# Optimization experiments

Hardware: AMD Instinct MI355X
Metric: run time of the kernel (lower is better)

## Reference

```python
import jax, jax.numpy as jnp
import numpy as np

NUM_EXPERTS = 8
TOP_K = 2
B, S, H = 4, 1024, 1024
FF = 2 * H  # expert hidden = 2*hidden_size per the torch code


def setup_inputs() -> dict:
    key = jax.random.key(0)
    ks = jax.random.split(key, 5)
    scale = 0.02
    return {
        "x": jax.random.normal(ks[0], (B, S, H), dtype=jnp.float32),
        "Wg": jax.random.normal(ks[1], (H, NUM_EXPERTS), dtype=jnp.float32) * scale,
        "bg": jnp.zeros((NUM_EXPERTS,), dtype=jnp.float32),
        "W1": jax.random.normal(ks[2], (NUM_EXPERTS, H, FF), dtype=jnp.float32) * scale,
        "b1": jnp.zeros((NUM_EXPERTS, FF), dtype=jnp.float32),
        "W2": jax.random.normal(ks[3], (NUM_EXPERTS, FF, H), dtype=jnp.float32) * scale,
        "b2": jnp.zeros((NUM_EXPERTS, H), dtype=jnp.float32),
    }


def reference(x, Wg, bg, W1, b1, W2, b2):
    b, s, h = x.shape
    xf = x.reshape(-1, h)  # [T, H]
    # Gating: softmax over experts, then top-k and renormalize (as in torch code)
    gate_scores = jax.nn.softmax(xf @ Wg + bg, axis=-1)  # [T, E]
    top_v, top_i = jax.lax.top_k(gate_scores, TOP_K)      # [T, K]
    top_v = top_v / jnp.sum(top_v, axis=-1, keepdims=True)
    # Combine weights per (token, expert): gate if expert selected else 0
    combine = jnp.sum(jax.nn.one_hot(top_i, NUM_EXPERTS, dtype=xf.dtype)
                      * top_v[..., None], axis=1)         # [T, E]
    # Dense all-expert MLP (eval-mode dropout = identity), then gated combine
    hmid = jax.nn.relu(jnp.einsum('th,ehf->tef', xf, W1) + b1)  # [T, E, FF]
    yexp = jnp.einsum('tef,efh->teh', hmid, W2) + b2            # [T, E, H]
    out = jnp.einsum('te,teh->th', combine, yexp)               # [T, H]
    return out.reshape(b, s, h)
```

## Files before the change

kernel.cpp:

```cpp
#include <hip/hip_runtime.h>
#include <hip/hip_bf16.h>

#define T_TOK 4096
#define HD    1024
#define FFD   2048
#define NE    8

typedef __attribute__((ext_vector_type(8))) short short8;
typedef __attribute__((ext_vector_type(4))) float f32x4;

__device__ __forceinline__ unsigned short f2bf(float f) {
  __hip_bfloat16 h = __float2bfloat16(f);
  return __builtin_bit_cast(unsigned short, h);
}

__device__ __forceinline__ void gload_lds16(const unsigned short* g, unsigned short* l) {
  __builtin_amdgcn_global_load_lds(
      (const __attribute__((address_space(1))) unsigned int*)g,
      (__attribute__((address_space(3))) unsigned int*)l, 16, 0, 0);
}

__global__ __launch_bounds__(256) void prep_kernel(
    const float* __restrict__ x, const float* __restrict__ Wg,
    const float* __restrict__ bg,
    const float* __restrict__ W1, const float* __restrict__ W2,
    int* __restrict__ top_i, float2* __restrict__ top_w,
    unsigned short* __restrict__ xbf,
    unsigned short* __restrict__ W1T, unsigned short* __restrict__ W2T,
    float* __restrict__ out)
{
  __shared__ float tile[64][69];
  const int bid = blockIdx.x;
  const int tid = threadIdx.x;

  if (bid < T_TOK / 4) {
    {
      size_t b = ((size_t)bid * 256 + tid) * 16;
      float4 z = make_float4(0.f, 0.f, 0.f, 0.f);
#pragma unroll
      for (int q = 0; q < 4; ++q) *(float4*)(out + b + q * 4) = z;
    }
    const int wave = tid >> 6;
    const int lane = tid & 63;
    const int t = bid * 4 + wave;

    float acc[NE];
#pragma unroll
    for (int e = 0; e < NE; ++e) acc[e] = 0.f;

    const float* xr = x + (size_t)t * HD;
    unsigned short* xo = xbf + (size_t)t * HD;
#pragma unroll
    for (int it = 0; it < 4; ++it) {
      const int h0 = lane * 4 + it * 256;
      float4 xv = *(const float4*)(xr + h0);
#pragma unroll
      for (int j = 0; j < 4; ++j) {
        float xs = (&xv.x)[j];
        float4 a = *(const float4*)(Wg + (size_t)(h0 + j) * NE);
        float4 b = *(const float4*)(Wg + (size_t)(h0 + j) * NE + 4);
        acc[0] = fmaf(xs, a.x, acc[0]); acc[1] = fmaf(xs, a.y, acc[1]);
        acc[2] = fmaf(xs, a.z, acc[2]); acc[3] = fmaf(xs, a.w, acc[3]);
        acc[4] = fmaf(xs, b.x, acc[4]); acc[5] = fmaf(xs, b.y, acc[5]);
        acc[6] = fmaf(xs, b.z, acc[6]); acc[7] = fmaf(xs, b.w, acc[7]);
      }
      ushort4 u;
      u.x = f2bf(xv.x); u.y = f2bf(xv.y); u.z = f2bf(xv.z); u.w = f2bf(xv.w);
      *(ushort4*)(xo + h0) = u;
    }
#pragma unroll
    for (int off = 32; off > 0; off >>= 1) {
#pragma unroll
      for (int e = 0; e < NE; ++e) acc[e] += __shfl_xor(acc[e], off);
    }
    if (lane == 0) {
      float lg[NE];
#pragma unroll
      for (int e = 0; e < NE; ++e) lg[e] = acc[e] + bg[e];
      int i1 = 0;
#pragma unroll
      for (int e = 1; e < NE; ++e) if (lg[e] > lg[i1]) i1 = e;
      int i2 = (i1 == 0) ? 1 : 0;
#pragma unroll
      for (int e = 0; e < NE; ++e) if (e != i1 && lg[e] > lg[i2]) i2 = e;
      float p2 = expf(lg[i2] - lg[i1]);
      float s  = 1.f + p2;
      top_i[t] = i1 | (i2 << 8);
      top_w[t] = make_float2(1.f / s, p2 / s);
    }
    return;
  }

  const float* in; unsigned short* ow; int R, C, idx;
  if (bid < T_TOK / 4 + 4096) {
    idx = bid - T_TOK / 4;          in = W1; ow = W1T; R = HD;  C = FFD;
  } else {
    idx = bid - (T_TOK / 4 + 4096); in = W2; ow = W2T; R = FFD; C = HD;
  }
  const int cpt = C >> 6, rpt = R >> 6;
  const int cx = idx % cpt;
  const int cy = (idx / cpt) % rpt;
  const int z  = idx / (cpt * rpt);
  const int r0 = cy * 64, c0 = cx * 64;

  const float* ip = in + ((size_t)z * R + r0) * C + c0;
  int tr = tid >> 4, tc = (tid & 15) * 4;
#pragma unroll
  for (int j = 0; j < 4; ++j) {
    float4 v = *(const float4*)(ip + (size_t)(tr + j * 16) * C + tc);
    float* tp = &tile[tr + j * 16][tc];
    tp[0] = v.x; tp[1] = v.y; tp[2] = v.z; tp[3] = v.w;
  }
  __syncthreads();
  unsigned short* op = ow + ((size_t)z * C + c0) * R + r0;
  int oc = tid >> 4, orr = (tid & 15) * 4;
#pragma unroll
  for (int j = 0; j < 4; ++j) {
    int c = oc + j * 16;
    ushort4 w;
    w.x = f2bf(tile[orr + 0][c]);
    w.y = f2bf(tile[orr + 1][c]);
    w.z = f2bf(tile[orr + 2][c]);
    w.w = f2bf(tile[orr + 3][c]);
    *(ushort4*)(op + (size_t)c * R + orr) = w;
  }
}

__global__ __launch_bounds__(256) void route_kernel(
    const int* __restrict__ top_i, const float2* __restrict__ top_w,
    int* __restrict__ counts, int* __restrict__ ids, float* __restrict__ wts)
{
  const int e   = blockIdx.x;
  const int tid = threadIdx.x;
  __shared__ int psum[256];

  const int t0 = tid * 16;
  unsigned int flags = 0;
  int cnt = 0;
#pragma unroll
  for (int j = 0; j < 16; ++j) {
    int ti = top_i[t0 + j];
    bool m = ((ti & 255) == e) || (((ti >> 8) & 255) == e);
    flags |= (m ? 1u : 0u) << j;
    cnt += m;
  }
  psum[tid] = cnt;
  __syncthreads();
  for (int off = 1; off < 256; off <<= 1) {
    int v = (tid >= off) ? psum[tid - off] : 0;
    __syncthreads();
    psum[tid] += v;
    __syncthreads();
  }
  int rank = psum[tid] - cnt;
#pragma unroll
  for (int j = 0; j < 16; ++j) {
    if (flags & (1u << j)) {
      int t = t0 + j;
      int ti = top_i[t];
      float2 w = top_w[t];
      ids[e * T_TOK + rank] = t;
      wts[e * T_TOK + rank] = ((ti & 255) == e) ? w.x : w.y;
      ++rank;
    }
  }
  if (tid == 255) counts[e] = psum[255];
}

template<int KD, int ND, int KSPLIT, bool G1M, bool GATHER_A>
__global__ __launch_bounds__(256, 4) void pair_gemm128_kernel(
    const unsigned short* __restrict__ A,
    const unsigned short* __restrict__ BT,
    const float* __restrict__ bias,
    const int* __restrict__ counts, const int* __restrict__ ids,
    const float* __restrict__ wts,
    unsigned short* __restrict__ Hout, float* __restrict__ out)
{
  constexpr int CT    = ND / 128;
  constexpr int KTILE = KD / KSPLIT;
  constexpr int NT    = KTILE / 64;
  constexpr int SPX   = 128;

  const int e  = blockIdx.x & 7;
  const int s0 = blockIdx.x >> 3;
  int cnt = 0, base = 0;
#pragma unroll
  for (int k = 0; k < NE; ++k) {
    int c = counts[k];
    if (k < e)  base += (c + 255) & ~255;
    if (k == e) cnt = c;
  }
  const int ntiles = (cnt + 127) >> 7;
  const int njobs  = ntiles * CT * KSPLIT;

  __shared__ __align__(16) unsigned short As[128 * 64];
  __shared__ __align__(16) unsigned short Bs[128 * 64];

  const int tid  = threadIdx.x;
  const int w    = tid >> 6;
  const int lane = tid & 63;
  const int g    = lane >> 4;
  const int rA   = lane & 15;
  const int wr   = w >> 1;
  const int wc   = w & 1;
  const int sw   = rA & 7;
  const int srow = lane >> 3;
  const int lc8  = ((lane & 7) ^ srow) * 8;

  for (int slot = s0; slot < njobs; slot += SPX) {
    const int rt   = slot % ntiles;
    const int ct   = (slot / ntiles) % CT;
    const int kp   = slot / (ntiles * CT);
    const int row0 = base + rt * 128;
    const int koff = kp * KTILE;

    const unsigned short* arow[4];
#pragma unroll
    for (int jj = 0; jj < 4; ++jj) {
      const int lrow = w * 32 + jj * 8 + srow;
      int src;
      if constexpr (GATHER_A) {
        int i = rt * 128 + lrow;
        src = ids[e * T_TOK + (i < cnt ? i : cnt - 1)];
      } else {
        src = row0 + lrow;
      }
      arow[jj] = A + (size_t)src * KD + koff + lc8;
    }
    const unsigned short* Bb =
        BT + ((size_t)e * ND + (size_t)ct * 128) * KD + koff + lc8;

    f32x4 acc[4][4];
#pragma unroll
    for (int mf = 0; mf < 4; ++mf)
#pragma unroll
      for (int nf = 0; nf < 4; ++nf)
        acc[mf][nf] = (f32x4){0.f, 0.f, 0.f, 0.f};

    for (int kc = 0; kc < KTILE; kc += 64) {
      __syncthreads();
#pragma unroll
      for (int jj = 0; jj < 4; ++jj) {
        const int rg = w * 32 + jj * 8;
        gload_lds16(arow[jj] + kc, &As[rg * 64]);
        gload_lds16(Bb + (size_t)(rg + srow) * KD + kc, &Bs[rg * 64]);
      }
      __syncthreads();
#pragma unroll
      for (int ks = 0; ks < 2; ++ks) {
        const int pc = ((ks * 4 + g) ^ sw) << 3;
        short8 af[4], bf[4];
#pragma unroll
        for (int mf = 0; mf < 4; ++mf)
          af[mf] = *(const short8*)&As[(wr * 64 + mf * 16 + rA) * 64 + pc];
#pragma unroll
        for (int nf = 0; nf < 4; ++nf)
          bf[nf] = *(const short8*)&Bs[(wc * 64 + nf * 16 + rA) * 64 + pc];
#pragma unroll
        for (int mf = 0; mf < 4; ++mf)
#pragma unroll
          for (int nf = 0; nf < 4; ++nf)
            acc[mf][nf] = __builtin_amdgcn_mfma_f32_16x16x32_bf16(
                af[mf], bf[nf], acc[mf][nf], 0, 0, 0);
      }
    }

    float bv[4];
#pragma unroll
    for (int nf = 0; nf < 4; ++nf)
      bv[nf] = (KSPLIT == 1 || kp == 0)
                   ? bias[e * ND + ct * 128 + wc * 64 + nf * 16 + rA] : 0.f;

    if constexpr (G1M) {
#pragma unroll
      for (int mf = 0; mf < 4; ++mf)
#pragma unroll
        for (int r = 0; r < 4; ++r) {
          const int row = row0 + wr * 64 + mf * 16 + g * 4 + r;
          unsigned short* hrow =
              Hout + (size_t)row * FFD + ct * 128 + wc * 64 + rA;
#pragma unroll
          for (int nf = 0; nf < 4; ++nf)
            hrow[nf * 16] = f2bf(fmaxf(acc[mf][nf][r] + bv[nf], 0.f));
        }
    } else {
#pragma unroll
      for (int mf = 0; mf < 4; ++mf)
#pragma unroll
        for (int r = 0; r < 4; ++r) {
          const int i = rt * 128 + wr * 64 + mf * 16 + g * 4 + r;
          if (i >= cnt) continue;
          const int tok = ids[e * T_TOK + i];
          const float wt = wts[e * T_TOK + i];
          float* orow = out + (size_t)tok * HD + ct * 128 + wc * 64 + rA;
#pragma unroll
          for (int nf = 0; nf < 4; ++nf)
            atomicAdd(&orow[nf * 16], wt * (acc[mf][nf][r] + bv[nf]));
        }
    }
  }
}

extern "C" void kernel_launch(void* const* d_in, const int* in_sizes, int n_in,
                              void* d_out, int out_size, void* d_ws, size_t ws_size,
                              hipStream_t stream) {
  const float* x  = (const float*)d_in[0];
  const float* Wg = (const float*)d_in[1];
  const float* bg = (const float*)d_in[2];
  const float* W1 = (const float*)d_in[3];
  const float* b1 = (const float*)d_in[4];
  const float* W2 = (const float*)d_in[5];
  const float* b2 = (const float*)d_in[6];
  float* out = (float*)d_out;

  const size_t OFF_TOPI = 512;
  const size_t OFF_TOPW = OFF_TOPI + (size_t)T_TOK * 4;
  const size_t OFF_IDS  = OFF_TOPW + (size_t)T_TOK * 8;
  const size_t OFF_WTS  = OFF_IDS + (size_t)T_TOK * NE * 4;
  const size_t OFF_XBF  = OFF_WTS + (size_t)T_TOK * NE * 4;
  const size_t OFF_W1T  = OFF_XBF + (size_t)T_TOK * HD * 2;
  const size_t OFF_W2T  = OFF_W1T + (size_t)NE * HD * FFD * 2;
  const size_t OFF_H    = OFF_W2T + (size_t)NE * HD * FFD * 2;
  const size_t REQ      = OFF_H + (size_t)10240 * FFD * 2;

  if (ws_size < REQ) return;

  int*            counts = (int*)d_ws;
  int*            top_i  = (int*)((char*)d_ws + OFF_TOPI);
  float2*         top_w  = (float2*)((char*)d_ws + OFF_TOPW);
  int*            ids    = (int*)((char*)d_ws + OFF_IDS);
  float*          wts    = (float*)((char*)d_ws + OFF_WTS);
  unsigned short* xbf    = (unsigned short*)((char*)d_ws + OFF_XBF);
  unsigned short* W1T    = (unsigned short*)((char*)d_ws + OFF_W1T);
  unsigned short* W2T    = (unsigned short*)((char*)d_ws + OFF_W2T);
  unsigned short* H      = (unsigned short*)((char*)d_ws + OFF_H);

  prep_kernel<<<T_TOK / 4 + 2 * 4096, 256, 0, stream>>>(
      x, Wg, bg, W1, W2, top_i, top_w, xbf, W1T, W2T, out);
  route_kernel<<<NE, 256, 0, stream>>>(top_i, top_w, counts, ids, wts);

  pair_gemm128_kernel<HD, FFD, 1, true, true>
      <<<NE * 128, 256, 0, stream>>>(xbf, W1T, b1, counts, ids, wts, H, nullptr);
  pair_gemm128_kernel<FFD, HD, 2, false, false>
      <<<NE * 128, 256, 0, stream>>>(H, W2T, b2, counts, ids, wts, nullptr, out);
}
```

Before: 192.2 us.

## Use 256x128 tiles with 512 threads and double-buffered LDS prefetch

The expert GEMM kernel now uses 512-thread blocks computing 256x128 output tiles, one job per block instead of a persistent grid-stride loop. LDS is double-buffered so the next K-slice's global-to-LDS loads are issued before the current slice's MFMAs, with a single barrier per iteration. The larger tile reuses each B tile across more rows, reducing global traffic, and the prefetch overlaps load latency with compute. In exchange, padding waste grows for experts whose token count is not a multiple of 256, LDS use rises to 96 KB per block, and occupancy falls to 2 blocks per CU.

```diff
diff --git a/kernel.cpp b/kernel.cpp
--- a/kernel.cpp
+++ b/kernel.cpp
@@ -168,7 +168,7 @@
 }
 
 template<int KD, int ND, int KSPLIT, bool G1M, bool GATHER_A>
-__global__ __launch_bounds__(256, 4) void pair_gemm128_kernel(
+__global__ __launch_bounds__(512, 2) void pair_gemm256_kernel(
     const unsigned short* __restrict__ A,
     const unsigned short* __restrict__ BT,
     const float* __restrict__ bias,
@@ -179,10 +179,9 @@
   constexpr int CT    = ND / 128;
   constexpr int KTILE = KD / KSPLIT;
   constexpr int NT    = KTILE / 64;
-  constexpr int SPX   = 128;
-
-  const int e  = blockIdx.x & 7;
-  const int s0 = blockIdx.x >> 3;
+
+  const int e    = blockIdx.x & 7;
+  const int slot = blockIdx.x >> 3;
   int cnt = 0, base = 0;
 #pragma unroll
   for (int k = 0; k < NE; ++k) {
@@ -190,11 +189,16 @@
     if (k < e)  base += (c + 255) & ~255;
     if (k == e) cnt = c;
   }
-  const int ntiles = (cnt + 127) >> 7;
-  const int njobs  = ntiles * CT * KSPLIT;
-
-  __shared__ __align__(16) unsigned short As[128 * 64];
-  __shared__ __align__(16) unsigned short Bs[128 * 64];
+  const int ntiles = (cnt + 255) >> 8;
+  if (slot >= ntiles * CT * KSPLIT) return;
+  const int rt   = slot % ntiles;
+  const int ct   = (slot / ntiles) % CT;
+  const int kp   = slot / (ntiles * CT);
+  const int row0 = base + rt * 256;
+  const int koff = kp * KTILE;
+
+  __shared__ __align__(16) unsigned short As[2][256 * 64];
+  __shared__ __align__(16) unsigned short Bs[2][128 * 64];
 
   const int tid  = threadIdx.x;
   const int w    = tid >> 6;
@@ -207,97 +211,106 @@
   const int srow = lane >> 3;
   const int lc8  = ((lane & 7) ^ srow) * 8;
 
-  for (int slot = s0; slot < njobs; slot += SPX) {
-    const int rt   = slot % ntiles;
-    const int ct   = (slot / ntiles) % CT;
-    const int kp   = slot / (ntiles * CT);
-    const int row0 = base + rt * 128;
-    const int koff = kp * KTILE;
-
-    const unsigned short* arow[4];
-#pragma unroll
-    for (int jj = 0; jj < 4; ++jj) {
-      const int lrow = w * 32 + jj * 8 + srow;
-      int src;
-      if constexpr (GATHER_A) {
-        int i = rt * 128 + lrow;
-        src = ids[e * T_TOK + (i < cnt ? i : cnt - 1)];
-      } else {
-        src = row0 + lrow;
+  const unsigned short* arow[4];
+#pragma unroll
+  for (int jj = 0; jj < 4; ++jj) {
+    const int lrow = w * 32 + jj * 8 + srow;
+    int src;
+    if constexpr (GATHER_A) {
+      int i = rt * 256 + lrow;
+      src = ids[e * T_TOK + (i < cnt ? i : cnt - 1)];
+    } else {
+      src = row0 + lrow;
+    }
+    arow[jj] = A + (size_t)src * KD + koff + lc8;
+  }
+  const unsigned short* brow[2];
+#pragma unroll
+  for (int jj = 0; jj < 2; ++jj) {
+    const int lrow = w * 16 + jj * 8 + srow;
+    brow[jj] = BT + ((size_t)e * ND + ct * 128 + lrow) * KD + koff + lc8;
+  }
+
+  f32x4 acc[4][4];
+#pragma unroll
+  for (int mf = 0; mf < 4; ++mf)
+#pragma unroll
+    for (int nf = 0; nf < 4; ++nf)
+      acc[mf][nf] = (f32x4){0.f, 0.f, 0.f, 0.f};
+
+  auto stage = [&](int buf, int kc) {
+#pragma unroll
+    for (int jj = 0; jj < 4; ++jj)
+      gload_lds16(arow[jj] + kc, &As[buf][(w * 32 + jj * 8) * 64]);
+#pragma unroll
+    for (int jj = 0; jj < 2; ++jj)
+      gload_lds16(brow[jj] + kc, &Bs[buf][(w * 16 + jj * 8) * 64]);
+  };
+
+  stage(0, 0);
+  asm volatile("s_waitcnt vmcnt(0)" ::: "memory");
+  __builtin_amdgcn_s_barrier();
+
+#pragma unroll 2
+  for (int t = 0; t < NT; ++t) {
+    const int cur = t & 1;
+    if (t + 1 < NT) stage(cur ^ 1, (t + 1) * 64);
+    __builtin_amdgcn_sched_barrier(0);
+
+#pragma unroll
+    for (int ks = 0; ks < 2; ++ks) {
+      const int pc = ((ks * 4 + g) ^ sw) << 3;
+      short8 bf[4];
+#pragma unroll
+      for (int nf = 0; nf < 4; ++nf)
+        bf[nf] = *(const short8*)&Bs[cur][(wc * 64 + nf * 16 + rA) * 64 + pc];
+#pragma unroll
+      for (int mf = 0; mf < 4; ++mf) {
+        short8 af = *(const short8*)&As[cur][(wr * 64 + mf * 16 + rA) * 64 + pc];
+#pragma unroll
+        for (int nf = 0; nf < 4; ++nf)
+          acc[mf][nf] = __builtin_amdgcn_mfma_f32_16x16x32_bf16(
+              af, bf[nf], acc[mf][nf], 0, 0, 0);
       }
-      arow[jj] = A + (size_t)src * KD + koff + lc8;
-    }
-    const unsigned short* Bb =
-        BT + ((size_t)e * ND + (size_t)ct * 128) * KD + koff + lc8;
-
-    f32x4 acc[4][4];
+    }
+
+    asm volatile("s_waitcnt lgkmcnt(0) vmcnt(0)" ::: "memory");
+    __builtin_amdgcn_sched_barrier(0);
+    __builtin_amdgcn_s_barrier();
+    __builtin_amdgcn_sched_barrier(0);
+  }
+
+  float bv[4];
+#pragma unroll
+  for (int nf = 0; nf < 4; ++nf)
+    bv[nf] = (KSPLIT == 1 || kp == 0)
+                 ? bias[e * ND + ct * 128 + wc * 64 + nf * 16 + rA] : 0.f;
+
+  if constexpr (G1M) {
 #pragma unroll
     for (int mf = 0; mf < 4; ++mf)
 #pragma unroll
-      for (int nf = 0; nf < 4; ++nf)
-        acc[mf][nf] = (f32x4){0.f, 0.f, 0.f, 0.f};
-
-    for (int kc = 0; kc < KTILE; kc += 64) {
-      __syncthreads();
-#pragma unroll
-      for (int jj = 0; jj < 4; ++jj) {
-        const int rg = w * 32 + jj * 8;
-        gload_lds16(arow[jj] + kc, &As[rg * 64]);
-        gload_lds16(Bb + (size_t)(rg + srow) * KD + kc, &Bs[rg * 64]);
+      for (int r = 0; r < 4; ++r) {
+        const int row = row0 + wr * 64 + mf * 16 + g * 4 + r;
+        unsigned short* hrow = Hout + (size_t)row * FFD + ct * 128 + wc * 64 + rA;
+#pragma unroll
+        for (int nf = 0; nf < 4; ++nf)
+          hrow[nf * 16] = f2bf(fmaxf(acc[mf][nf][r] + bv[nf], 0.f));
       }
-      __syncthreads();
-#pragma unroll
-      for (int ks = 0; ks < 2; ++ks) {
-        const int pc = ((ks * 4 + g) ^ sw) << 3;
-        short8 af[4], bf[4];
-#pragma unroll
-        for (int mf = 0; mf < 4; ++mf)
-          af[mf] = *(const short8*)&As[(wr * 64 + mf * 16 + rA) * 64 + pc];
+  } else {
+#pragma unroll
+    for (int mf = 0; mf < 4; ++mf)
+#pragma unroll
+      for (int r = 0; r < 4; ++r) {
+        const int i = rt * 256 + wr * 64 + mf * 16 + g * 4 + r;
+        if (i >= cnt) continue;
+        const int tok = ids[e * T_TOK + i];
+        const float wt = wts[e * T_TOK + i];
+        float* orow = out + (size_t)tok * HD + ct * 128 + wc * 64 + rA;
 #pragma unroll
         for (int nf = 0; nf < 4; ++nf)
-          bf[nf] = *(const short8*)&Bs[(wc * 64 + nf * 16 + rA) * 64 + pc];
-#pragma unroll
-        for (int mf = 0; mf < 4; ++mf)
-#pragma unroll
-          for (int nf = 0; nf < 4; ++nf)
-            acc[mf][nf] = __builtin_amdgcn_mfma_f32_16x16x32_bf16(
-                af[mf], bf[nf], acc[mf][nf], 0, 0, 0);
+          atomicAdd(&orow[nf * 16], wt * (acc[mf][nf][r] + bv[nf]));
       }
-    }
-
-    float bv[4];
-#pragma unroll
-    for (int nf = 0; nf < 4; ++nf)
-      bv[nf] = (KSPLIT == 1 || kp == 0)
-                   ? bias[e * ND + ct * 128 + wc * 64 + nf * 16 + rA] : 0.f;
-
-    if constexpr (G1M) {
-#pragma unroll
-      for (int mf = 0; mf < 4; ++mf)
-#pragma unroll
-        for (int r = 0; r < 4; ++r) {
-          const int row = row0 + wr * 64 + mf * 16 + g * 4 + r;
-          unsigned short* hrow =
-              Hout + (size_t)row * FFD + ct * 128 + wc * 64 + rA;
-#pragma unroll
-          for (int nf = 0; nf < 4; ++nf)
-            hrow[nf * 16] = f2bf(fmaxf(acc[mf][nf][r] + bv[nf], 0.f));
-        }
-    } else {
-#pragma unroll
-      for (int mf = 0; mf < 4; ++mf)
-#pragma unroll
-        for (int r = 0; r < 4; ++r) {
-          const int i = rt * 128 + wr * 64 + mf * 16 + g * 4 + r;
-          if (i >= cnt) continue;
-          const int tok = ids[e * T_TOK + i];
-          const float wt = wts[e * T_TOK + i];
-          float* orow = out + (size_t)tok * HD + ct * 128 + wc * 64 + rA;
-#pragma unroll
-          for (int nf = 0; nf < 4; ++nf)
-            atomicAdd(&orow[nf * 16], wt * (acc[mf][nf][r] + bv[nf]));
-        }
-    }
   }
 }
 
@@ -339,8 +352,8 @@
       x, Wg, bg, W1, W2, top_i, top_w, xbf, W1T, W2T, out);
   route_kernel<<<NE, 256, 0, stream>>>(top_i, top_w, counts, ids, wts);
 
-  pair_gemm128_kernel<HD, FFD, 1, true, true>
-      <<<NE * 128, 256, 0, stream>>>(xbf, W1T, b1, counts, ids, wts, H, nullptr);
-  pair_gemm128_kernel<FFD, HD, 2, false, false>
-      <<<NE * 128, 256, 0, stream>>>(H, W2T, b2, counts, ids, wts, nullptr, out);
-}
+  pair_gemm256_kernel<HD, FFD, 1, true, true>
+      <<<NE * 256, 512, 0, stream>>>(xbf, W1T, b1, counts, ids, wts, H, nullptr);
+  pair_gemm256_kernel<FFD, HD, 2, false, false>
+      <<<NE * 256, 512, 0, stream>>>(H, W2T, b2, counts, ids, wts, nullptr, out);
+}
```

Result: slower. 235.7 us (+22.6%).

## Replace persistent slot loop with one-tile-per-block grid and drop split-K

Applied to the files above, without the earlier changes.

The GEMM kernels stop looping over job slots in a persistent grid of 1024 blocks. Each block now computes exactly one output tile, with the grid sized to an upper bound and excess blocks exiting early. Split-K for the second GEMM is removed, so each output element gets one atomicAdd instead of two, but each block runs a K loop twice as long. The change targets loop overhead and imbalance across slots, at the cost of launching more, mostly idle, blocks.

```diff
diff --git a/kernel.cpp b/kernel.cpp
--- a/kernel.cpp
+++ b/kernel.cpp
@@ -167,7 +167,7 @@
   if (tid == 255) counts[e] = psum[255];
 }
 
-template<int KD, int ND, int KSPLIT, bool G1M, bool GATHER_A>
+template<int KD, int ND, bool G1M, bool GATHER_A>
 __global__ __launch_bounds__(256, 4) void pair_gemm128_kernel(
     const unsigned short* __restrict__ A,
     const unsigned short* __restrict__ BT,
@@ -176,13 +176,10 @@
     const float* __restrict__ wts,
     unsigned short* __restrict__ Hout, float* __restrict__ out)
 {
-  constexpr int CT    = ND / 128;
-  constexpr int KTILE = KD / KSPLIT;
-  constexpr int NT    = KTILE / 64;
-  constexpr int SPX   = 128;
-
-  const int e  = blockIdx.x & 7;
-  const int s0 = blockIdx.x >> 3;
+  constexpr int CT = ND / 128;
+
+  const int e    = blockIdx.x & 7;
+  const int slot = blockIdx.x >> 3;
   int cnt = 0, base = 0;
 #pragma unroll
   for (int k = 0; k < NE; ++k) {
@@ -191,7 +188,10 @@
     if (k == e) cnt = c;
   }
   const int ntiles = (cnt + 127) >> 7;
-  const int njobs  = ntiles * CT * KSPLIT;
+  if (slot >= ntiles * CT) return;
+  const int rt   = slot % ntiles;
+  const int ct   = slot / ntiles;
+  const int row0 = base + rt * 128;
 
   __shared__ __align__(16) unsigned short As[128 * 64];
   __shared__ __align__(16) unsigned short Bs[128 * 64];
@@ -207,97 +207,86 @@
   const int srow = lane >> 3;
   const int lc8  = ((lane & 7) ^ srow) * 8;
 
-  for (int slot = s0; slot < njobs; slot += SPX) {
-    const int rt   = slot % ntiles;
-    const int ct   = (slot / ntiles) % CT;
-    const int kp   = slot / (ntiles * CT);
-    const int row0 = base + rt * 128;
-    const int koff = kp * KTILE;
-
-    const unsigned short* arow[4];
+  const unsigned short* arow[4];
+#pragma unroll
+  for (int jj = 0; jj < 4; ++jj) {
+    const int lrow = w * 32 + jj * 8 + srow;
+    int src;
+    if constexpr (GATHER_A) {
+      int i = rt * 128 + lrow;
+      src = ids[e * T_TOK + (i < cnt ? i : cnt - 1)];
+    } else {
+      src = row0 + lrow;
+    }
+    arow[jj] = A + (size_t)src * KD + lc8;
+  }
+  const unsigned short* Bb = BT + ((size_t)e * ND + (size_t)ct * 128) * KD + lc8;
+
+  f32x4 acc[4][4];
+#pragma unroll
+  for (int mf = 0; mf < 4; ++mf)
+#pragma unroll
+    for (int nf = 0; nf < 4; ++nf)
+      acc[mf][nf] = (f32x4){0.f, 0.f, 0.f, 0.f};
+
+  for (int kc = 0; kc < KD; kc += 64) {
+    __syncthreads();
 #pragma unroll
     for (int jj = 0; jj < 4; ++jj) {
-      const int lrow = w * 32 + jj * 8 + srow;
-      int src;
-      if constexpr (GATHER_A) {
-        int i = rt * 128 + lrow;
-        src = ids[e * T_TOK + (i < cnt ? i : cnt - 1)];
-      } else {
-        src = row0 + lrow;
+      const int rg = w * 32 + jj * 8;
+      gload_lds16(arow[jj] + kc, &As[rg * 64]);
+      gload_lds16(Bb + (size_t)(rg + srow) * KD + kc, &Bs[rg * 64]);
+    }
+    __syncthreads();
+#pragma unroll
+    for (int ks = 0; ks < 2; ++ks) {
+      const int pc = ((ks * 4 + g) ^ sw) << 3;
+      short8 af[4], bf[4];
+#pragma unroll
+      for (int mf = 0; mf < 4; ++mf)
+        af[mf] = *(const short8*)&As[(wr * 64 + mf * 16 + rA) * 64 + pc];
+#pragma unroll
+      for (int nf = 0; nf < 4; ++nf)
+        bf[nf] = *(const short8*)&Bs[(wc * 64 + nf * 16 + rA) * 64 + pc];
+#pragma unroll
+      for (int mf = 0; mf < 4; ++mf)
+#pragma unroll
+        for (int nf = 0; nf < 4; ++nf)
+          acc[mf][nf] = __builtin_amdgcn_mfma_f32_16x16x32_bf16(
+              af[mf], bf[nf], acc[mf][nf], 0, 0, 0);
+    }
+  }
+
+  float bv[4];
+#pragma unroll
+  for (int nf = 0; nf < 4; ++nf)
+    bv[nf] = bias[e * ND + ct * 128 + wc * 64 + nf * 16 + rA];
+
+  if constexpr (G1M) {
+#pragma unroll
+    for (int mf = 0; mf < 4; ++mf)
+#pragma unroll
+      for (int r = 0; r < 4; ++r) {
+        const int row = row0 + wr * 64 + mf * 16 + g * 4 + r;
+        unsigned short* hrow = Hout + (size_t)row * FFD + ct * 128 + wc * 64 + rA;
+#pragma unroll
+        for (int nf = 0; nf < 4; ++nf)
+          hrow[nf * 16] = f2bf(fmaxf(acc[mf][nf][r] + bv[nf], 0.f));
       }
-      arow[jj] = A + (size_t)src * KD + koff + lc8;
-    }
-    const unsigned short* Bb =
-        BT + ((size_t)e * ND + (size_t)ct * 128) * KD + koff + lc8;
-
-    f32x4 acc[4][4];
+  } else {
 #pragma unroll
     for (int mf = 0; mf < 4; ++mf)
 #pragma unroll
-      for (int nf = 0; nf < 4; ++nf)
-        acc[mf][nf] = (f32x4){0.f, 0.f, 0.f, 0.f};
-
-    for (int kc = 0; kc < KTILE; kc += 64) {
-      __syncthreads();
-#pragma unroll
-      for (int jj = 0; jj < 4; ++jj) {
-        const int rg = w * 32 + jj * 8;
-        gload_lds16(arow[jj] + kc, &As[rg * 64]);
-        gload_lds16(Bb + (size_t)(rg + srow) * KD + kc, &Bs[rg * 64]);
+      for (int r = 0; r < 4; ++r) {
+        const int i = rt * 128 + wr * 64 + mf * 16 + g * 4 + r;
+        if (i >= cnt) continue;
+        const int tok = ids[e * T_TOK + i];
+        const float wt = wts[e * T_TOK + i];
+        float* orow = out + (size_t)tok * HD + ct * 128 + wc * 64 + rA;
+#pragma unroll
+        for (int nf = 0; nf < 4; ++nf)
+          atomicAdd(&orow[nf * 16], wt * (acc[mf][nf][r] + bv[nf]));
       }
-      __syncthreads();
-#pragma unroll
-      for (int ks = 0; ks < 2; ++ks) {
-        const int pc = ((ks * 4 + g) ^ sw) << 3;
-        short8 af[4], bf[4];
-#pragma unroll
-        for (int mf = 0; mf < 4; ++mf)
-          af[mf] = *(const short8*)&As[(wr * 64 + mf * 16 + rA) * 64 + pc];
-#pragma unroll
-        for (int nf = 0; nf < 4; ++nf)
-          bf[nf] = *(const short8*)&Bs[(wc * 64 + nf * 16 + rA) * 64 + pc];
-#pragma unroll
-        for (int mf = 0; mf < 4; ++mf)
-#pragma unroll
-          for (int nf = 0; nf < 4; ++nf)
-            acc[mf][nf] = __builtin_amdgcn_mfma_f32_16x16x32_bf16(
-                af[mf], bf[nf], acc[mf][nf], 0, 0, 0);
-      }
-    }
-
-    float bv[4];
-#pragma unroll
-    for (int nf = 0; nf < 4; ++nf)
-      bv[nf] = (KSPLIT == 1 || kp == 0)
-                   ? bias[e * ND + ct * 128 + wc * 64 + nf * 16 + rA] : 0.f;
-
-    if constexpr (G1M) {
-#pragma unroll
-      for (int mf = 0; mf < 4; ++mf)
-#pragma unroll
-        for (int r = 0; r < 4; ++r) {
-          const int row = row0 + wr * 64 + mf * 16 + g * 4 + r;
-          unsigned short* hrow =
-              Hout + (size_t)row * FFD + ct * 128 + wc * 64 + rA;
-#pragma unroll
-          for (int nf = 0; nf < 4; ++nf)
-            hrow[nf * 16] = f2bf(fmaxf(acc[mf][nf][r] + bv[nf], 0.f));
-        }
-    } else {
-#pragma unroll
-      for (int mf = 0; mf < 4; ++mf)
-#pragma unroll
-        for (int r = 0; r < 4; ++r) {
-          const int i = rt * 128 + wr * 64 + mf * 16 + g * 4 + r;
-          if (i >= cnt) continue;
-          const int tok = ids[e * T_TOK + i];
-          const float wt = wts[e * T_TOK + i];
-          float* orow = out + (size_t)tok * HD + ct * 128 + wc * 64 + rA;
-#pragma unroll
-          for (int nf = 0; nf < 4; ++nf)
-            atomicAdd(&orow[nf * 16], wt * (acc[mf][nf][r] + bv[nf]));
-        }
-    }
   }
 }
 
@@ -339,8 +328,8 @@
       x, Wg, bg, W1, W2, top_i, top_w, xbf, W1T, W2T, out);
   route_kernel<<<NE, 256, 0, stream>>>(top_i, top_w, counts, ids, wts);
 
-  pair_gemm128_kernel<HD, FFD, 1, true, true>
-      <<<NE * 128, 256, 0, stream>>>(xbf, W1T, b1, counts, ids, wts, H, nullptr);
-  pair_gemm128_kernel<FFD, HD, 2, false, false>
-      <<<NE * 128, 256, 0, stream>>>(H, W2T, b2, counts, ids, wts, nullptr, out);
-}
+  pair_gemm128_kernel<HD, FFD, true, true>
+      <<<NE * 512, 256, 0, stream>>>(xbf, W1T, b1, counts, ids, wts, H, nullptr);
+  pair_gemm128_kernel<FFD, HD, false, false>
+      <<<NE * 256, 256, 0, stream>>>(H, W2T, b2, counts, ids, wts, nullptr, out);
+}
```

After: 171.2 us. 10.9% less time.
